# Kernel optimization log

Measured on AMD Instinct MI355X. Metric: run time of the kernel, lower is better.

Reference implementation:

```python
import jax, jax.numpy as jnp
import numpy as np

B, S, T = 16, 400, 51
V, E, H = 50000, 128, 256
MAX_OOV = 50
EXT = V + MAX_OOV
COV_LOSS_WEIGHT = 1.0


def setup_inputs() -> dict:
    key = jax.random.key(0)
    ks = jax.random.split(key, 24)
    sc = 0.05  # param scale
    inp = {
        "tgt": jax.random.randint(ks[0], (B, T), 0, V, dtype=jnp.int32),
        "hidden": jax.random.normal(ks[1], (1, B, H), jnp.float32),
        "cell": jax.random.normal(ks[2], (1, B, H), jnp.float32),
        "encoder_outputs": jax.random.normal(ks[3], (B, S, H), jnp.float32),
        "src_lens": jax.random.randint(ks[4], (B,), S // 2, S + 1, dtype=jnp.int32),
        "src_ids": jax.random.randint(ks[5], (B, S), 0, V, dtype=jnp.int32),
        # -1 means in-vocab token; >=0 means OOV slot index (max MAX_OOV-1)
        "src_oov_map": jax.random.randint(ks[6], (B, S), -1, MAX_OOV, dtype=jnp.int32),
        "embedding": jax.random.normal(ks[7], (V, E), jnp.float32) * sc,
        "W_h": jax.random.normal(ks[8], (H, H), jnp.float32) * sc,
        "W_s": jax.random.normal(ks[9], (H, H), jnp.float32) * sc,
        "w_c": jax.random.normal(ks[10], (H,), jnp.float32) * sc,
        "v": jax.random.normal(ks[11], (H,), jnp.float32) * sc,
        "b_attn": jnp.zeros((1,), jnp.float32),
        "W_ih": jax.random.normal(ks[12], (4 * H, E + H), jnp.float32) * sc,
        "W_hh": jax.random.normal(ks[13], (4 * H, H), jnp.float32) * sc,
        "b_ih": jax.random.normal(ks[14], (4 * H,), jnp.float32) * sc,
        "b_hh": jax.random.normal(ks[15], (4 * H,), jnp.float32) * sc,
        "W_pg": jax.random.normal(ks[16], (1, 2 * H + E), jnp.float32) * sc,
        "b_pg": jnp.zeros((1,), jnp.float32),
        "W_out": jax.random.normal(ks[17], (V, 2 * H), jnp.float32) * sc,
        "b_out": jnp.zeros((V,), jnp.float32),
    }
    return inp


def reference(tgt, hidden, cell, encoder_outputs, src_lens, src_ids, src_oov_map,
              embedding, W_h, W_s, w_c, v, b_attn,
              W_ih, W_hh, b_ih, b_hh, W_pg, b_pg, W_out, b_out):
    # Precompute encoder projection and masks (loop-invariant)
    Wh_h = jnp.einsum('bsh,kh->bsk', encoder_outputs, W_h)        # [B,S,H]
    pad_mask = jnp.arange(S)[None, :] >= src_lens[:, None]       # [B,S]
    copy_idx = jnp.where(src_oov_map >= 0, V + src_oov_map, src_ids)  # [B,S]
    batch_idx = jnp.arange(B)[:, None]

    def step(carry, y_prev):
        h, c, cov = carry                                       # [B,H],[B,H],[B,S]
        emb = embedding[y_prev]                                 # [B,E]
        # coverage attention (additive, See et al. 2017 eq. 9-11)
        attn_in = Wh_h + (h @ W_s.T)[:, None, :] + cov[..., None] * w_c + b_attn
        scores = jnp.tanh(attn_in) @ v                          # [B,S]
        scores = jnp.where(pad_mask, -1e9, scores)
        attn = jax.nn.softmax(scores, axis=1)                   # [B,S]
        context = jnp.einsum('bs,bsh->bh', attn, encoder_outputs)
        cov_loss = jnp.sum(jnp.minimum(attn, cov), axis=1)      # [B]
        # single-layer LSTM cell (torch gate order i,f,g,o)
        x = jnp.concatenate([emb, context], axis=1)             # [B,E+H]
        gates = x @ W_ih.T + h @ W_hh.T + b_ih + b_hh
        i, f, g, o = jnp.split(gates, 4, axis=1)
        c_new = jax.nn.sigmoid(f) * c + jax.nn.sigmoid(i) * jnp.tanh(g)
        h_new = jax.nn.sigmoid(o) * jnp.tanh(c_new)
        # pointer-generator mixture
        p_gen = jax.nn.sigmoid(
            jnp.concatenate([h_new, context, emb], axis=1) @ W_pg.T + b_pg)  # [B,1]
        logits = jnp.concatenate([h_new, context], axis=1) @ W_out.T + b_out
        vocab_dist = jax.nn.softmax(logits, axis=1)             # [B,V]
        ext_dist = jnp.pad(vocab_dist, ((0, 0), (0, MAX_OOV)))  # [B,EXT]
        copy_dist = jnp.zeros((B, EXT), vocab_dist.dtype).at[batch_idx, copy_idx].add(attn)
        final = p_gen * ext_dist + (1.0 - p_gen) * copy_dist
        return (h_new, c_new, cov + attn), (final, cov_loss)

    carry0 = (hidden[0], cell[0], jnp.zeros((B, S), jnp.float32))
    # teacher forcing: decoder input at step t is tgt[:, t-1], t = 1..T-1
    (hT, cT, _), (dists, cov_losses) = jax.lax.scan(step, carry0, tgt[:, :-1].T)
    all_dists = jnp.transpose(dists, (1, 0, 2))                 # [B,T-1,EXT]
    coverage_loss = COV_LOSS_WEIGHT * jnp.mean(cov_losses)
    return all_dists, hT[None], cT[None], coverage_loss
```

## Files before the change

kernel.cpp:

```cpp
#include <hip/hip_runtime.h>
#include <math.h>

#define CB 16
#define CS 400
#define CT 51
#define CTM1 50
#define CV 50000
#define CE 128
#define CH 256
#define CMAXOOV 50
#define CEXT (CV + CMAXOOV)
#define CX 640
#define NST 16
#define NGT 16
#define NWK 223
#define NBLK 256
#define NTILE 782

typedef __attribute__((ext_vector_type(4))) float f32x4;
typedef __attribute__((ext_vector_type(8))) short short8;
typedef unsigned int U32;
typedef unsigned long long U64;

__device__ __forceinline__ float wave_sum(float x) {
#pragma unroll
  for (int o = 32; o > 0; o >>= 1) x += __shfl_xor(x, o);
  return x;
}
__device__ __forceinline__ float sigm(float x) {
  return 1.f / (1.f + __expf(-x));
}
__device__ __forceinline__ float ftanh(float x) {
  x = fminf(fmaxf(x, -15.f), 15.f);
  float e = __expf(2.f * x);
  return (e - 1.f) / (e + 1.f);
}
__device__ __forceinline__ unsigned short f2bf(float f) {
  union { float f; U32 u; } x;
  x.f = f;
  U32 r = x.u + 0x7FFFu + ((x.u >> 16) & 1u);
  return (unsigned short)(r >> 16);
}
__device__ __forceinline__ float bf2f(unsigned short u) {
  return __uint_as_float(((U32)u) << 16);
}
__device__ __forceinline__ U64 pack4(float a, float b, float c, float d) {
  return (U64)f2bf(a) | ((U64)f2bf(b) << 16) | ((U64)f2bf(c) << 32) |
         ((U64)f2bf(d) << 48);
}
__device__ __forceinline__ U32 ald32(const U32* p) {
  return __hip_atomic_load(p, __ATOMIC_RELAXED, __HIP_MEMORY_SCOPE_AGENT);
}
__device__ __forceinline__ void ast32(U32* p, U32 v) {
  __hip_atomic_store(p, v, __ATOMIC_RELAXED, __HIP_MEMORY_SCOPE_AGENT);
}
__device__ __forceinline__ void ast64(U64* p, U64 v) {
  __hip_atomic_store(p, v, __ATOMIC_RELAXED, __HIP_MEMORY_SCOPE_AGENT);
}
#define VM0 asm volatile("s_waitcnt vmcnt(0)" ::: "memory")

__global__ __launch_bounds__(256) void pw_convert(
    const float* __restrict__ W, unsigned short* __restrict__ Wb) {
  size_t i = ((size_t)blockIdx.x * 256 + threadIdx.x) * 8;
  float4 a = *(const float4*)(W + i);
  float4 b = *(const float4*)(W + i + 4);
  short8 o;
  o[0] = (short)f2bf(a.x); o[1] = (short)f2bf(a.y);
  o[2] = (short)f2bf(a.z); o[3] = (short)f2bf(a.w);
  o[4] = (short)f2bf(b.x); o[5] = (short)f2bf(b.y);
  o[6] = (short)f2bf(b.z); o[7] = (short)f2bf(b.w);
  *(short8*)(Wb + i) = o;
}

__global__ __launch_bounds__(256) void pw_cat(
    const float* __restrict__ W_ih, const float* __restrict__ W_hh,
    unsigned short* __restrict__ Wcat) {
  int t8 = blockIdx.x * 256 + threadIdx.x;
  int j = t8 / 80, k8 = t8 % 80;
  short8 o;
#pragma unroll
  for (int i = 0; i < 8; ++i) {
    int k = k8 * 8 + i;
    float v = (k < CE + CH) ? W_ih[(size_t)j * (CE + CH) + k]
                            : W_hh[(size_t)j * CH + (k - (CE + CH))];
    o[i] = (short)f2bf(v);
  }
  *(short8*)(Wcat + (size_t)t8 * 8) = o;
}

__global__ __launch_bounds__(256) void pw_t256(const float* __restrict__ in,
                                               float* __restrict__ out) {
  int j = blockIdx.x, k = threadIdx.x;
  out[j * CH + k] = in[k * CH + j];
}

__global__ __launch_bounds__(256) void pw_t256_bf16(
    const float* __restrict__ in, unsigned short* __restrict__ out) {
  int j = blockIdx.x, k = threadIdx.x;
  out[j * CH + k] = f2bf(in[k * CH + j]);
}

__global__ __launch_bounds__(256) void pw_cvt16(
    const float* __restrict__ in, unsigned short* __restrict__ out) {
  size_t i = ((size_t)blockIdx.x * 256 + threadIdx.x) * 8;
  float4 a = *(const float4*)(in + i);
  float4 b = *(const float4*)(in + i + 4);
  short8 o;
  o[0] = (short)f2bf(a.x); o[1] = (short)f2bf(a.y);
  o[2] = (short)f2bf(a.z); o[3] = (short)f2bf(a.w);
  o[4] = (short)f2bf(b.x); o[5] = (short)f2bf(b.y);
  o[6] = (short)f2bf(b.z); o[7] = (short)f2bf(b.w);
  *(short8*)(out + i) = o;
}

__global__ __launch_bounds__(256) void p0_precompute(
    const float* __restrict__ enc, const float* __restrict__ W_hT,
    const int* __restrict__ src_ids, const int* __restrict__ src_oov,
    unsigned short* __restrict__ Wh_h16, int* __restrict__ copy_idx) {
  const int row0 = blockIdx.x * 8, tid = threadIdx.x;
  __shared__ float erT[CH * 8];
#pragma unroll
  for (int i = 0; i < 8; ++i) {
    int idx = tid + i * 256;
    int r = idx >> 8, j = idx & 255;
    erT[j * 8 + r] = enc[(size_t)row0 * CH + idx];
  }
  if (tid < 8) {
    int row = row0 + tid;
    int ov = src_oov[row];
    copy_idx[row] = (ov >= 0) ? (CV + ov) : src_ids[row];
  }
  __syncthreads();
  float acc[8] = {0, 0, 0, 0, 0, 0, 0, 0};
#pragma unroll 4
  for (int j = 0; j < CH; ++j) {
    float w = W_hT[j * CH + tid];
    float4 e0 = *(const float4*)&erT[j * 8];
    float4 e1 = *(const float4*)&erT[j * 8 + 4];
    acc[0] += e0.x * w; acc[1] += e0.y * w; acc[2] += e0.z * w; acc[3] += e0.w * w;
    acc[4] += e1.x * w; acc[5] += e1.y * w; acc[6] += e1.z * w; acc[7] += e1.w * w;
  }
#pragma unroll
  for (int r = 0; r < 8; ++r)
    Wh_h16[(size_t)(row0 + r) * CH + tid] = f2bf(acc[r]);
}

__global__ __launch_bounds__(256) void z_init(U32* __restrict__ ctrl,
                                              float* __restrict__ part) {
  int tid = blockIdx.x * 256 + threadIdx.x;
  if (tid < 2048) ctrl[tid] = 0u;
  for (int i = tid; i < CTM1 * CB * 64; i += 256 * 64) part[i] = 0.f;
}

__global__ __launch_bounds__(1024, 4) void mega(
    const int* __restrict__ tgt, const float* __restrict__ hidden,
    const float* __restrict__ cell, const int* __restrict__ src_lens,
    const float* __restrict__ embedding, const float* __restrict__ w_c,
    const float* __restrict__ v_vec, const float* __restrict__ b_attn,
    const float* __restrict__ b_ih, const float* __restrict__ b_hh,
    const float* __restrict__ W_pg, const float* __restrict__ b_pg,
    const float* __restrict__ b_out,
    const unsigned short* __restrict__ Wh_h16,
    const unsigned short* __restrict__ enc16,
    const unsigned short* __restrict__ W_sT16,
    const unsigned short* __restrict__ Wcat,
    const unsigned short* __restrict__ Wb, U64* __restrict__ A64,
    U64* __restrict__ x64, U64* __restrict__ g64,
    unsigned short* __restrict__ attn16, float* __restrict__ p_gen_g,
    float* __restrict__ part, float* __restrict__ covloss_b,
    U32* __restrict__ ctrl, float* __restrict__ dout) {
  const int bid = blockIdx.x, tid = threadIdx.x;
  const int lane = tid & 63, wv = tid >> 6;
  U32* arrive = ctrl;
  U32* release = ctrl + 256;
  U32* xrdy = ctrl + 1280;
  U32* grdy = ctrl + 1536;

  __shared__ __align__(16) U64 sh_big[2592];
  __shared__ float cov_s[CS];
  __shared__ float a_s[CS];
  __shared__ __align__(16) float h_cur[CH];
  __shared__ float hws_s[CH];
  __shared__ __align__(16) float ctx_s[CH];
  __shared__ float emb_s[CE];
  __shared__ float pctx[4 * CH];
  __shared__ float gsl[CB][64];
  __shared__ float red[16];
  __shared__ float stat[4];
  __shared__ float prs[16][16];

  if (bid < NST) {
    const int b = bid;
    const int len = src_lens[b];
    const float ba = b_attn[0];
    const int k4 = lane * 4;
    const float4 wc4 = *(const float4*)(w_c + k4);
    const float4 vv4 = *(const float4*)(v_vec + k4);
    const float bias_reg = b_ih[tid] + b_hh[tid];
    const int kg = tid & 255, grp = tid >> 8;
    float covl = 0.f;
    float c_reg = (tid < CH) ? cell[b * CH + tid] : 0.f;

    if (tid < CS) cov_s[tid] = 0.f;
    if (tid < CH) h_cur[tid] = hidden[b * CH + tid];
    __syncthreads();
    {
      float acc = 0.f;
#pragma unroll 8
      for (int j = grp * 64; j < grp * 64 + 64; ++j)
        acc += h_cur[j] * bf2f(W_sT16[j * CH + kg]);
      pctx[grp * CH + kg] = acc;
    }
    if (tid < 64)
      ast64(&x64[b * 160 + 96 + tid],
            pack4(h_cur[4 * tid], h_cur[4 * tid + 1], h_cur[4 * tid + 2],
                  h_cur[4 * tid + 3]));
    __syncthreads();
    if (tid < CH)
      hws_s[tid] = pctx[tid] + pctx[CH + tid] + pctx[2 * CH + tid] +
                   pctx[3 * CH + tid];
    __syncthreads();

    for (int t = 0; t < CTM1; ++t) {
      if (t > 0) {
        if (tid < CS) {
          float a = a_s[tid], cv = cov_s[tid];
          covl += fminf(a, cv);
          cov_s[tid] = cv + a;
        }
        __syncthreads();
      }
      const int tok = tgt[b * CT + t];
      if (tid < CE) emb_s[tid] = embedding[(size_t)tok * CE + tid];
      float ps = 0.f;
      for (int s = wv; s < CS; s += 16) {
        float cv = cov_s[s];
        U64 wq = *(const U64*)(Wh_h16 + ((size_t)(b * CS + s)) * CH + k4);
        float p =
            ftanh(bf2f((unsigned short)wq) + hws_s[k4] + cv * wc4.x + ba) *
                vv4.x +
            ftanh(bf2f((unsigned short)(wq >> 16)) + hws_s[k4 + 1] +
                  cv * wc4.y + ba) *
                vv4.y +
            ftanh(bf2f((unsigned short)(wq >> 32)) + hws_s[k4 + 2] +
                  cv * wc4.z + ba) *
                vv4.z +
            ftanh(bf2f((unsigned short)(wq >> 48)) + hws_s[k4 + 3] +
                  cv * wc4.w + ba) *
                vv4.w;
        p = wave_sum(p);
        if (lane == 0) {
          float e = (s < len) ? __expf(p) : 0.f;
          a_s[s] = e;
          ps += e;
        }
      }
      if (lane == 0) red[wv] = ps;
      __syncthreads();
      if (tid == 0) {
        float s2 = 0.f;
#pragma unroll
        for (int i = 0; i < 16; ++i) s2 += red[i];
        stat[0] = 1.f / s2;
      }
      __syncthreads();
      const float inv = stat[0];
      if (tid < CS) {
        float a = a_s[tid] * inv;
        a_s[tid] = a;
        attn16[((size_t)t * CB + b) * CS + tid] = f2bf(a);
      }
      __syncthreads();
      {
        float pc = 0.f;
        const unsigned short* er =
            enc16 + ((size_t)(b * CS + grp * 100)) * CH + kg;
#pragma unroll 10
        for (int i = 0; i < 100; ++i)
          pc += a_s[grp * 100 + i] * bf2f(er[(size_t)i * CH]);
        pctx[grp * CH + kg] = pc;
      }
      __syncthreads();
      if (tid < CH)
        ctx_s[tid] = pctx[tid] + pctx[CH + tid] + pctx[2 * CH + tid] +
                     pctx[3 * CH + tid];
      __syncthreads();
      {
        U64* xr = x64 + (size_t)t * 2560 + b * 160;
        if (tid < 32) {
          ast64(&xr[tid], pack4(emb_s[4 * tid], emb_s[4 * tid + 1],
                                emb_s[4 * tid + 2], emb_s[4 * tid + 3]));
        } else if (tid < 96) {
          int i = tid - 32;
          ast64(&xr[32 + i], pack4(ctx_s[4 * i], ctx_s[4 * i + 1],
                                   ctx_s[4 * i + 2], ctx_s[4 * i + 3]));
        } else if (tid < 160) {
          int i = tid - 96;
          ast64(&A64[(size_t)t * 2048 + b * 128 + 64 + i],
                pack4(ctx_s[4 * i], ctx_s[4 * i + 1], ctx_s[4 * i + 2],
                      ctx_s[4 * i + 3]));
        }
      }
      VM0;
      __syncthreads();
      if (tid == 0) ast32(&xrdy[b * 16], (U32)(t + 1));
      if (wv == 0) {
        int gg = 0;
        while (gg < (1 << 20)) {
          U32 v = (lane < NGT) ? ald32(&grdy[lane * 16]) : (U32)(t + 1);
          if (__all(v >= (U32)(t + 1))) break;
          __builtin_amdgcn_s_sleep(4);
          ++gg;
        }
      }
      __syncthreads();
      if (tid < CH) {
        const float* gr = (const float*)(g64 + (size_t)t * 8192) + b * 1024;
        float gi = gr[tid] + bias_reg;
        float gf = gr[CH + tid] + b_ih[CH + tid] + b_hh[CH + tid];
        float gg2 = gr[2 * CH + tid] + b_ih[2 * CH + tid] + b_hh[2 * CH + tid];
        float go = gr[3 * CH + tid] + b_ih[3 * CH + tid] + b_hh[3 * CH + tid];
        float cn = sigm(gf) * c_reg + sigm(gi) * ftanh(gg2);
        c_reg = cn;
        h_cur[tid] = sigm(go) * ftanh(cn);
      }
      __syncthreads();
      if (tid < 64) {
        ast64(&A64[(size_t)t * 2048 + b * 128 + tid],
              pack4(h_cur[4 * tid], h_cur[4 * tid + 1], h_cur[4 * tid + 2],
                    h_cur[4 * tid + 3]));
      } else if (tid < 128 && t + 1 < CTM1) {
        int i = tid - 64;
        ast64(&x64[(size_t)(t + 1) * 2560 + b * 160 + 96 + i],
              pack4(h_cur[4 * i], h_cur[4 * i + 1], h_cur[4 * i + 2],
                    h_cur[4 * i + 3]));
      }
      VM0;
      __syncthreads();
      if (tid == 0) ast32(&arrive[b * 16], (U32)(t + 1));
      {
        float acc = 0.f;
#pragma unroll 8
        for (int j = grp * 64; j < grp * 64 + 64; ++j)
          acc += h_cur[j] * bf2f(W_sT16[j * CH + kg]);
        pctx[grp * CH + kg] = acc;
      }
      __syncthreads();
      if (tid < CH)
        hws_s[tid] = pctx[tid] + pctx[CH + tid] + pctx[2 * CH + tid] +
                     pctx[3 * CH + tid];
      {
        float z = 0.f;
        if (tid < CH)
          z = h_cur[tid] * W_pg[tid] + ctx_s[tid] * W_pg[CH + tid];
        if (tid < CE) z += emb_s[tid] * W_pg[2 * CH + tid];
        z = wave_sum(z);
        if (lane == 0) red[wv] = z;
        __syncthreads();
        if (tid == 0) {
          float s2 = 0.f;
#pragma unroll
          for (int i = 0; i < 16; ++i) s2 += red[i];
          p_gen_g[t * CB + b] = sigm(s2 + b_pg[0]);
        }
      }
      __syncthreads();
    }
    if (tid < CS) covl += fminf(a_s[tid], cov_s[tid]);
    covl = wave_sum(covl);
    if (lane == 0) red[wv] = covl;
    __syncthreads();
    if (tid == 0) {
      float s2 = 0.f;
#pragma unroll
      for (int i = 0; i < 16; ++i) s2 += red[i];
      covloss_b[b] = s2;
    }
    if (tid < CH) {
      const size_t D0 = (size_t)CB * CTM1 * CEXT;
      dout[D0 + b * CH + tid] = h_cur[tid];
      dout[D0 + CB * CH + b * CH + tid] = c_reg;
    }
  } else if (bid < NST + NGT) {
    const int g = bid - NST;
    const int n0 = g * 64;
    const int nn = lane & 15, gq = lane >> 4;
    U64* xl = sh_big;
    const short8* x8 = (const short8*)sh_big;
    for (int t = 0; t < CTM1; ++t) {
      if (wv == 0) {
        int gg = 0;
        while (gg < (1 << 20)) {
          U32 v = (lane < NST) ? ald32(&xrdy[lane * 16]) : (U32)(t + 1);
          if (__all(v >= (U32)(t + 1))) break;
          __builtin_amdgcn_s_sleep(4);
          ++gg;
        }
      }
      __syncthreads();
      {
        const U64* src = x64 + (size_t)t * 2560;
        for (int idx = tid; idx < 2560; idx += 1024) {
          int row = idx / 160, col = idx - row * 160;
          xl[row * 162 + col] = src[idx];
        }
      }
      __syncthreads();
      if (wv < 4) {
        const int ncol = n0 + wv * 16 + nn;
        const short8* bp = (const short8*)Wcat + (size_t)ncol * 80;
        short8 af[20];
#pragma unroll
        for (int kt = 0; kt < 20; ++kt) af[kt] = x8[nn * 81 + kt * 4 + gq];
        f32x4 acc = {0.f, 0.f, 0.f, 0.f};
#pragma unroll
        for (int kt = 0; kt < 20; ++kt)
          acc = __builtin_amdgcn_mfma_f32_16x16x32_bf16(af[kt], bp[kt * 4 + gq],
                                                        acc, 0, 0, 0);
#pragma unroll
        for (int r = 0; r < 4; ++r) gsl[gq * 4 + r][wv * 16 + nn] = acc[r];
      }
      __syncthreads();
      if (tid < 512) {
        int b = tid >> 5, i = tid & 31;
        U64 w = (U64)__float_as_uint(gsl[b][2 * i]) |
                ((U64)__float_as_uint(gsl[b][2 * i + 1]) << 32);
        ast64(&g64[(size_t)t * 8192 + b * 512 + (n0 >> 1) + i], w);
      }
      VM0;
      __syncthreads();
      if (tid == 0) ast32(&grdy[g * 16], (U32)(t + 1));
    }
  } else if (bid == NST + NGT) {
    for (int t = 0; t < CTM1; ++t) {
      if (wv == 0) {
        int gg = 0;
        while (gg < (1 << 20)) {
          U32 v = (lane < NST) ? ald32(&arrive[lane * 16]) : (U32)(t + 1);
          if (__all(v >= (U32)(t + 1))) break;
          __builtin_amdgcn_s_sleep(8);
          ++gg;
        }
      }
      __syncthreads();
      if (tid < 64) ast32(&release[tid * 16], (U32)(t + 1));
      __syncthreads();
    }
  } else {
    const int vb = bid - NST - NGT - 1;
    const int rep = vb & 63;
    const int nn = lane & 15, g = lane >> 4;
    const int t4 = (wv >> 2) * NWK + vb;
    const int v = t4 * 64 + (wv & 3) * 16 + nn;
    const bool live = (t4 < NTILE) && (v < CV);
    const int vc = live ? v : CV - 1;
    U64* a64l = sh_big;
    const short8* lds8 = (const short8*)sh_big;
    const short8* bp = (const short8*)Wb + (size_t)vc * 64;
    const float bo = live ? b_out[v] : 0.f;
    for (int t = 0; t < CTM1; ++t) {
      if (tid == 0) {
        int gg = 0;
        while (ald32(&release[rep * 16]) < (U32)(t + 1) && ++gg < (1 << 18))
          __builtin_amdgcn_s_sleep(32);
      }
      __syncthreads();
      {
        const U64* src = A64 + (size_t)t * 2048;
#pragma unroll
        for (int i = 0; i < 2; ++i) {
          int idx = tid + i * 1024;
          int row = idx >> 7, col = idx & 127;
          a64l[row * 130 + col] = src[idx];
        }
      }
      __syncthreads();
      short8 af[16];
#pragma unroll
      for (int kt = 0; kt < 16; ++kt) af[kt] = lds8[nn * 65 + kt * 4 + g];
      f32x4 acc = {0.f, 0.f, 0.f, 0.f};
#pragma unroll
      for (int kt = 0; kt < 16; ++kt)
        acc = __builtin_amdgcn_mfma_f32_16x16x32_bf16(af[kt], bp[kt * 4 + g],
                                                      acc, 0, 0, 0);
      float ev[4];
#pragma unroll
      for (int r = 0; r < 4; ++r) {
        float e = live ? __expf(acc[r] + bo) : 0.f;
        if (live) dout[((size_t)((g * 4 + r) * CTM1 + t)) * CEXT + v] = e;
#pragma unroll
        for (int o = 1; o < 16; o <<= 1) e += __shfl_xor(e, o);
        ev[r] = e;
      }
      if (nn == 0) {
#pragma unroll
        for (int r = 0; r < 4; ++r) prs[wv][g * 4 + r] = ev[r];
      }
      __syncthreads();
      if (tid < 16) {
        float s = 0.f;
#pragma unroll
        for (int w = 0; w < 16; ++w) s += prs[w][tid];
        atomicAdd(&part[((size_t)t * CB + tid) * 64 + rep], s);
      }
      __syncthreads();
    }
  }
}

__global__ __launch_bounds__(256) void post_norm(
    const float* __restrict__ part, const float* __restrict__ p_gen_g,
    float* __restrict__ dout) {
  const int R = blockIdx.x;
  const int b = R / CTM1, t = R % CTM1;
  const int tid = threadIdx.x;
  __shared__ float stat;
  float s = (tid < 64) ? part[((size_t)t * CB + b) * 64 + tid] : 0.f;
  s = wave_sum(s);
  if (tid == 0) stat = p_gen_g[t * CB + b] / s;
  __syncthreads();
  float inv = stat;
  float* drow = dout + (size_t)R * CEXT;
  for (int v = tid; v < CEXT; v += 256)
    drow[v] = (v < CV) ? drow[v] * inv : 0.f;
}

__global__ __launch_bounds__(256) void post_tail(
    const unsigned short* __restrict__ attn16,
    const float* __restrict__ p_gen_g, const int* __restrict__ copy_idx,
    const float* __restrict__ covloss_b, float* __restrict__ dout) {
  const int b = blockIdx.x, tid = threadIdx.x;
  for (int t = 0; t < CTM1; ++t) {
    float pg1 = 1.f - p_gen_g[t * CB + b];
    const unsigned short* ar = attn16 + ((size_t)t * CB + b) * CS;
    float* drow = dout + ((size_t)(b * CTM1 + t)) * CEXT;
    for (int s = tid; s < CS; s += 256)
      atomicAdd(drow + copy_idx[b * CS + s], pg1 * bf2f(ar[s]));
  }
  if (b == 0 && tid == 0) {
    const size_t D0 = (size_t)CB * CTM1 * CEXT;
    float s = 0.f;
    for (int i = 0; i < CB; ++i) s += covloss_b[i];
    dout[D0 + 2 * CB * CH] = s / (float)(CTM1 * CB);
  }
}

extern "C" void kernel_launch(void* const* d_in, const int* in_sizes, int n_in,
                              void* d_out, int out_size, void* d_ws,
                              size_t ws_size, hipStream_t stream) {
  const int* tgt = (const int*)d_in[0];
  const float* hidden = (const float*)d_in[1];
  const float* cell = (const float*)d_in[2];
  const float* enc = (const float*)d_in[3];
  const int* src_lens = (const int*)d_in[4];
  const int* src_ids = (const int*)d_in[5];
  const int* src_oov = (const int*)d_in[6];
  const float* embedding = (const float*)d_in[7];
  const float* W_h = (const float*)d_in[8];
  const float* W_s = (const float*)d_in[9];
  const float* w_c = (const float*)d_in[10];
  const float* v_vec = (const float*)d_in[11];
  const float* b_attn = (const float*)d_in[12];
  const float* W_ih = (const float*)d_in[13];
  const float* W_hh = (const float*)d_in[14];
  const float* b_ih = (const float*)d_in[15];
  const float* b_hh = (const float*)d_in[16];
  const float* W_pg = (const float*)d_in[17];
  const float* b_pg = (const float*)d_in[18];
  const float* W_out = (const float*)d_in[19];
  const float* b_out = (const float*)d_in[20];
  float* dout = (float*)d_out;

  float* ws = (float*)d_ws;
  float* W_hT = ws;
  float* p_gen_g = W_hT + CH * CH;
  float* part = p_gen_g + CTM1 * CB;
  float* covloss_b = part + CTM1 * CB * 64;
  int* copy_idx = (int*)(covloss_b + 16);
  U32* ctrl = (U32*)(copy_idx + CB * CS);
  U64* A64 = (U64*)(ctrl + 2048);
  U64* x64 = A64 + (size_t)CTM1 * 2048;
  U64* g64 = x64 + (size_t)51 * 2560;
  unsigned short* attn16 =
      (unsigned short*)(g64 + (size_t)CTM1 * 8192);
  unsigned short* Wh_h16 = attn16 + (size_t)CTM1 * CB * CS;
  unsigned short* enc16 = Wh_h16 + (size_t)CB * CS * CH;
  unsigned short* W_sT16 = enc16 + (size_t)CB * CS * CH;
  unsigned short* Wcat = W_sT16 + CH * CH;
  unsigned short* Wb = Wcat + (size_t)(4 * CH) * CX;

  z_init<<<64, 256, 0, stream>>>(ctrl, part);
  pw_convert<<<(CV * 2 * CH) / (256 * 8), 256, 0, stream>>>(W_out, Wb);
  pw_cat<<<((4 * CH) * CX / 8) / 256, 256, 0, stream>>>(W_ih, W_hh, Wcat);
  pw_t256<<<CH, CH, 0, stream>>>(W_h, W_hT);
  pw_t256_bf16<<<CH, CH, 0, stream>>>(W_s, W_sT16);
  pw_cvt16<<<(CB * CS * CH) / (256 * 8), 256, 0, stream>>>(enc, enc16);
  p0_precompute<<<CB * CS / 8, 256, 0, stream>>>(enc, W_hT, src_ids, src_oov,
                                                 Wh_h16, copy_idx);

  void* kargs[] = {
      (void*)&tgt,      (void*)&hidden,    (void*)&cell,    (void*)&src_lens,
      (void*)&embedding,(void*)&w_c,       (void*)&v_vec,   (void*)&b_attn,
      (void*)&b_ih,     (void*)&b_hh,      (void*)&W_pg,    (void*)&b_pg,
      (void*)&b_out,    (void*)&Wh_h16,    (void*)&enc16,   (void*)&W_sT16,
      (void*)&Wcat,     (void*)&Wb,        (void*)&A64,     (void*)&x64,
      (void*)&g64,      (void*)&attn16,    (void*)&p_gen_g, (void*)&part,
      (void*)&covloss_b,(void*)&ctrl,      (void*)&dout};
  hipError_t e = hipLaunchCooperativeKernel((const void*)mega, dim3(NBLK),
                                            dim3(1024), kargs, 0, stream);
  if (e != hipSuccess) {
    hipLaunchKernelGGL(mega, dim3(NBLK), dim3(1024), 0, stream, tgt, hidden,
                       cell, src_lens, embedding, w_c, v_vec, b_attn, b_ih,
                       b_hh, W_pg, b_pg, b_out, Wh_h16, enc16, W_sT16, Wcat,
                       Wb, A64, x64, g64, attn16, p_gen_g, part, covloss_b,
                       ctrl, dout);
  }
  post_norm<<<CB * CTM1, 256, 0, stream>>>(part, p_gen_g, dout);
  post_tail<<<CB, 256, 0, stream>>>(attn16, p_gen_g, copy_idx, covloss_b,
                                    dout);
}
```

Baseline: 2.003 ms.

## Move LSTM cell update into gate blocks and split gate GEMM around context wait

The LSTM cell nonlinearity and state update move from the per-batch attention blocks into the gate-GEMM blocks. Gate columns are reassigned so each block owns all four gates for 16 hidden units. The gate GEMM is split so the embedding and hidden parts are computed before waiting for the context, which overlaps them with attention work. Gate outputs go straight to h (HexF/A64) instead of a g64 round trip, removing one cross-block handoff per step, and the spin-wait sleeps are shortened. In exchange, gate blocks wait on each other's previous step and every gate block reloads embeddings itself.

```diff
diff --git a/kernel.cpp b/kernel.cpp
--- a/kernel.cpp
+++ b/kernel.cpp
@@ -165,13 +165,12 @@
     const unsigned short* __restrict__ W_sT16,
     const unsigned short* __restrict__ Wcat,
     const unsigned short* __restrict__ Wb, U64* __restrict__ A64,
-    U64* __restrict__ x64, U64* __restrict__ g64,
-    unsigned short* __restrict__ attn16, float* __restrict__ p_gen_g,
-    float* __restrict__ part, float* __restrict__ covloss_b,
-    U32* __restrict__ ctrl, float* __restrict__ dout) {
+    float* __restrict__ HexF, unsigned short* __restrict__ attn16,
+    float* __restrict__ p_gen_g, float* __restrict__ part,
+    float* __restrict__ covloss_b, U32* __restrict__ ctrl,
+    float* __restrict__ dout) {
   const int bid = blockIdx.x, tid = threadIdx.x;
   const int lane = tid & 63, wv = tid >> 6;
-  U32* arrive = ctrl;
   U32* release = ctrl + 256;
   U32* xrdy = ctrl + 1280;
   U32* grdy = ctrl + 1536;
@@ -184,7 +183,8 @@
   __shared__ __align__(16) float ctx_s[CH];
   __shared__ float emb_s[CE];
   __shared__ float pctx[4 * CH];
-  __shared__ float gsl[CB][64];
+  __shared__ float gsl[4][CB][16];
+  __shared__ int sh_tok[CB];
   __shared__ float red[16];
   __shared__ float stat[4];
   __shared__ float prs[16][16];
@@ -196,10 +196,8 @@
     const int k4 = lane * 4;
     const float4 wc4 = *(const float4*)(w_c + k4);
     const float4 vv4 = *(const float4*)(v_vec + k4);
-    const float bias_reg = b_ih[tid] + b_hh[tid];
     const int kg = tid & 255, grp = tid >> 8;
     float covl = 0.f;
-    float c_reg = (tid < CH) ? cell[b * CH + tid] : 0.f;
 
     if (tid < CS) cov_s[tid] = 0.f;
     if (tid < CH) h_cur[tid] = hidden[b * CH + tid];
@@ -211,10 +209,6 @@
         acc += h_cur[j] * bf2f(W_sT16[j * CH + kg]);
       pctx[grp * CH + kg] = acc;
     }
-    if (tid < 64)
-      ast64(&x64[b * 160 + 96 + tid],
-            pack4(h_cur[4 * tid], h_cur[4 * tid + 1], h_cur[4 * tid + 2],
-                  h_cur[4 * tid + 3]));
     __syncthreads();
     if (tid < CH)
       hws_s[tid] = pctx[tid] + pctx[CH + tid] + pctx[2 * CH + tid] +
@@ -230,8 +224,6 @@
         }
         __syncthreads();
       }
-      const int tok = tgt[b * CT + t];
-      if (tid < CE) emb_s[tid] = embedding[(size_t)tok * CE + tid];
       float ps = 0.f;
       for (int s = wv; s < CS; s += 16) {
         float cv = cov_s[s];
@@ -285,59 +277,28 @@
         ctx_s[tid] = pctx[tid] + pctx[CH + tid] + pctx[2 * CH + tid] +
                      pctx[3 * CH + tid];
       __syncthreads();
-      {
-        U64* xr = x64 + (size_t)t * 2560 + b * 160;
-        if (tid < 32) {
-          ast64(&xr[tid], pack4(emb_s[4 * tid], emb_s[4 * tid + 1],
-                                emb_s[4 * tid + 2], emb_s[4 * tid + 3]));
-        } else if (tid < 96) {
-          int i = tid - 32;
-          ast64(&xr[32 + i], pack4(ctx_s[4 * i], ctx_s[4 * i + 1],
-                                   ctx_s[4 * i + 2], ctx_s[4 * i + 3]));
-        } else if (tid < 160) {
-          int i = tid - 96;
-          ast64(&A64[(size_t)t * 2048 + b * 128 + 64 + i],
-                pack4(ctx_s[4 * i], ctx_s[4 * i + 1], ctx_s[4 * i + 2],
-                      ctx_s[4 * i + 3]));
-        }
+      if (tid < 64) {
+        ast64(&A64[(size_t)t * 2048 + b * 128 + 64 + tid],
+              pack4(ctx_s[4 * tid], ctx_s[4 * tid + 1], ctx_s[4 * tid + 2],
+                    ctx_s[4 * tid + 3]));
       }
       VM0;
       __syncthreads();
       if (tid == 0) ast32(&xrdy[b * 16], (U32)(t + 1));
+      if (tid < CE)
+        emb_s[tid] = embedding[(size_t)tgt[b * CT + t] * CE + tid];
       if (wv == 0) {
         int gg = 0;
-        while (gg < (1 << 20)) {
+        while (gg < (1 << 22)) {
           U32 v = (lane < NGT) ? ald32(&grdy[lane * 16]) : (U32)(t + 1);
           if (__all(v >= (U32)(t + 1))) break;
-          __builtin_amdgcn_s_sleep(4);
+          __builtin_amdgcn_s_sleep(1);
           ++gg;
         }
       }
       __syncthreads();
-      if (tid < CH) {
-        const float* gr = (const float*)(g64 + (size_t)t * 8192) + b * 1024;
-        float gi = gr[tid] + bias_reg;
-        float gf = gr[CH + tid] + b_ih[CH + tid] + b_hh[CH + tid];
-        float gg2 = gr[2 * CH + tid] + b_ih[2 * CH + tid] + b_hh[2 * CH + tid];
-        float go = gr[3 * CH + tid] + b_ih[3 * CH + tid] + b_hh[3 * CH + tid];
-        float cn = sigm(gf) * c_reg + sigm(gi) * ftanh(gg2);
-        c_reg = cn;
-        h_cur[tid] = sigm(go) * ftanh(cn);
-      }
-      __syncthreads();
-      if (tid < 64) {
-        ast64(&A64[(size_t)t * 2048 + b * 128 + tid],
-              pack4(h_cur[4 * tid], h_cur[4 * tid + 1], h_cur[4 * tid + 2],
-                    h_cur[4 * tid + 3]));
-      } else if (tid < 128 && t + 1 < CTM1) {
-        int i = tid - 64;
-        ast64(&x64[(size_t)(t + 1) * 2560 + b * 160 + 96 + i],
-              pack4(h_cur[4 * i], h_cur[4 * i + 1], h_cur[4 * i + 2],
-                    h_cur[4 * i + 3]));
-      }
-      VM0;
-      __syncthreads();
-      if (tid == 0) ast32(&arrive[b * 16], (U32)(t + 1));
+      if (tid < CH) h_cur[tid] = HexF[((size_t)t * CB + b) * CH + tid];
+      __syncthreads();
       {
         float acc = 0.f;
 #pragma unroll 8
@@ -379,66 +340,122 @@
     if (tid < CH) {
       const size_t D0 = (size_t)CB * CTM1 * CEXT;
       dout[D0 + b * CH + tid] = h_cur[tid];
-      dout[D0 + CB * CH + b * CH + tid] = c_reg;
     }
   } else if (bid < NST + NGT) {
     const int g = bid - NST;
-    const int n0 = g * 64;
     const int nn = lane & 15, gq = lane >> 4;
-    U64* xl = sh_big;
+    U64* xg64 = sh_big;
+    short* xg_s = (short*)sh_big;
     const short8* x8 = (const short8*)sh_big;
+    const int cb = tid >> 4, cj = tid & 15, cu = g * 16 + (tid & 15);
+    float c_reg = 0.f, bi0 = 0.f, bi1 = 0.f, bi2 = 0.f, bi3 = 0.f;
+    if (tid < 256) {
+      c_reg = cell[cb * CH + cu];
+      bi0 = b_ih[cu] + b_hh[cu];
+      bi1 = b_ih[CH + cu] + b_hh[CH + cu];
+      bi2 = b_ih[2 * CH + cu] + b_hh[2 * CH + cu];
+      bi3 = b_ih[3 * CH + cu] + b_hh[3 * CH + cu];
+    }
     for (int t = 0; t < CTM1; ++t) {
+      if (t > 0 && wv == 0) {
+        int gg = 0;
+        while (gg < (1 << 22)) {
+          U32 v = (lane < NGT) ? ald32(&grdy[lane * 16]) : (U32)t;
+          if (__all(v >= (U32)t)) break;
+          __builtin_amdgcn_s_sleep(1);
+          ++gg;
+        }
+      }
+      if (tid < CB) sh_tok[tid] = tgt[tid * CT + t];
+      __syncthreads();
+      for (int idx = tid; idx < CB * CE; idx += 1024) {
+        int bb = idx >> 7, k = idx & 127;
+        xg_s[bb * 648 + k] = (short)f2bf(embedding[(size_t)sh_tok[bb] * CE + k]);
+      }
+      if (t == 0) {
+        for (int idx = tid; idx < CB * CH; idx += 1024) {
+          int bb = idx >> 8, k = idx & 255;
+          xg_s[bb * 648 + 384 + k] = (short)f2bf(hidden[bb * CH + k]);
+        }
+      } else {
+        if (tid < 1024) {
+          int bb = tid >> 6, i = tid & 63;
+          xg64[bb * 162 + 96 + i] = A64[(size_t)(t - 1) * 2048 + bb * 128 + i];
+        }
+      }
+      __syncthreads();
+      f32x4 acc = {0.f, 0.f, 0.f, 0.f};
+      if (wv < 4) {
+        const int ncol = wv * 256 + g * 16 + nn;
+        const short8* bp = (const short8*)Wcat + (size_t)ncol * 80;
+#pragma unroll
+        for (int kt = 0; kt < 4; ++kt)
+          acc = __builtin_amdgcn_mfma_f32_16x16x32_bf16(
+              x8[nn * 81 + kt * 4 + gq], bp[kt * 4 + gq], acc, 0, 0, 0);
+#pragma unroll
+        for (int kt = 12; kt < 20; ++kt)
+          acc = __builtin_amdgcn_mfma_f32_16x16x32_bf16(
+              x8[nn * 81 + kt * 4 + gq], bp[kt * 4 + gq], acc, 0, 0, 0);
+      }
       if (wv == 0) {
         int gg = 0;
-        while (gg < (1 << 20)) {
+        while (gg < (1 << 22)) {
           U32 v = (lane < NST) ? ald32(&xrdy[lane * 16]) : (U32)(t + 1);
           if (__all(v >= (U32)(t + 1))) break;
-          __builtin_amdgcn_s_sleep(4);
+          __builtin_amdgcn_s_sleep(1);
           ++gg;
         }
       }
       __syncthreads();
-      {
-        const U64* src = x64 + (size_t)t * 2560;
-        for (int idx = tid; idx < 2560; idx += 1024) {
-          int row = idx / 160, col = idx - row * 160;
-          xl[row * 162 + col] = src[idx];
-        }
+      if (tid < 1024) {
+        int bb = tid >> 6, i = tid & 63;
+        xg64[bb * 162 + 32 + i] = A64[(size_t)t * 2048 + bb * 128 + 64 + i];
       }
       __syncthreads();
       if (wv < 4) {
-        const int ncol = n0 + wv * 16 + nn;
+        const int ncol = wv * 256 + g * 16 + nn;
         const short8* bp = (const short8*)Wcat + (size_t)ncol * 80;
-        short8 af[20];
-#pragma unroll
-        for (int kt = 0; kt < 20; ++kt) af[kt] = x8[nn * 81 + kt * 4 + gq];
-        f32x4 acc = {0.f, 0.f, 0.f, 0.f};
-#pragma unroll
-        for (int kt = 0; kt < 20; ++kt)
-          acc = __builtin_amdgcn_mfma_f32_16x16x32_bf16(af[kt], bp[kt * 4 + gq],
-                                                        acc, 0, 0, 0);
-#pragma unroll
-        for (int r = 0; r < 4; ++r) gsl[gq * 4 + r][wv * 16 + nn] = acc[r];
-      }
-      __syncthreads();
-      if (tid < 512) {
-        int b = tid >> 5, i = tid & 31;
-        U64 w = (U64)__float_as_uint(gsl[b][2 * i]) |
-                ((U64)__float_as_uint(gsl[b][2 * i + 1]) << 32);
-        ast64(&g64[(size_t)t * 8192 + b * 512 + (n0 >> 1) + i], w);
+#pragma unroll
+        for (int kt = 4; kt < 12; ++kt)
+          acc = __builtin_amdgcn_mfma_f32_16x16x32_bf16(
+              x8[nn * 81 + kt * 4 + gq], bp[kt * 4 + gq], acc, 0, 0, 0);
+#pragma unroll
+        for (int r = 0; r < 4; ++r) gsl[wv][gq * 4 + r][nn] = acc[r];
+      }
+      __syncthreads();
+      if (tid < 256) {
+        float gi = gsl[0][cb][cj] + bi0;
+        float gf = gsl[1][cb][cj] + bi1;
+        float gg2 = gsl[2][cb][cj] + bi2;
+        float go = gsl[3][cb][cj] + bi3;
+        float cn = sigm(gf) * c_reg + sigm(gi) * ftanh(gg2);
+        c_reg = cn;
+        float hn = sigm(go) * ftanh(cn);
+        ast32((U32*)&HexF[((size_t)t * CB + cb) * CH + cu],
+              __float_as_uint(hn));
+        float h1 = __shfl_down(hn, 1);
+        float h2 = __shfl_down(hn, 2);
+        float h3 = __shfl_down(hn, 3);
+        if (!(cj & 3))
+          ast64(&A64[(size_t)t * 2048 + cb * 128 + (cu >> 2)],
+                pack4(hn, h1, h2, h3));
       }
       VM0;
       __syncthreads();
       if (tid == 0) ast32(&grdy[g * 16], (U32)(t + 1));
+    }
+    if (tid < 256) {
+      const size_t D0 = (size_t)CB * CTM1 * CEXT;
+      dout[D0 + CB * CH + cb * CH + cu] = c_reg;
     }
   } else if (bid == NST + NGT) {
     for (int t = 0; t < CTM1; ++t) {
       if (wv == 0) {
         int gg = 0;
-        while (gg < (1 << 20)) {
-          U32 v = (lane < NST) ? ald32(&arrive[lane * 16]) : (U32)(t + 1);
+        while (gg < (1 << 22)) {
+          U32 v = (lane < NGT) ? ald32(&grdy[lane * 16]) : (U32)(t + 1);
           if (__all(v >= (U32)(t + 1))) break;
-          __builtin_amdgcn_s_sleep(8);
+          __builtin_amdgcn_s_sleep(4);
           ++gg;
         }
       }
@@ -576,13 +593,12 @@
   float* p_gen_g = W_hT + CH * CH;
   float* part = p_gen_g + CTM1 * CB;
   float* covloss_b = part + CTM1 * CB * 64;
-  int* copy_idx = (int*)(covloss_b + 16);
+  float* HexF = covloss_b + 16;
+  int* copy_idx = (int*)(HexF + (size_t)CTM1 * CB * CH);
   U32* ctrl = (U32*)(copy_idx + CB * CS);
   U64* A64 = (U64*)(ctrl + 2048);
-  U64* x64 = A64 + (size_t)CTM1 * 2048;
-  U64* g64 = x64 + (size_t)51 * 2560;
   unsigned short* attn16 =
-      (unsigned short*)(g64 + (size_t)CTM1 * 8192);
+      (unsigned short*)(A64 + (size_t)CTM1 * 2048);
   unsigned short* Wh_h16 = attn16 + (size_t)CTM1 * CB * CS;
   unsigned short* enc16 = Wh_h16 + (size_t)CB * CS * CH;
   unsigned short* W_sT16 = enc16 + (size_t)CB * CS * CH;
@@ -603,17 +619,17 @@
       (void*)&embedding,(void*)&w_c,       (void*)&v_vec,   (void*)&b_attn,
       (void*)&b_ih,     (void*)&b_hh,      (void*)&W_pg,    (void*)&b_pg,
       (void*)&b_out,    (void*)&Wh_h16,    (void*)&enc16,   (void*)&W_sT16,
-      (void*)&Wcat,     (void*)&Wb,        (void*)&A64,     (void*)&x64,
-      (void*)&g64,      (void*)&attn16,    (void*)&p_gen_g, (void*)&part,
-      (void*)&covloss_b,(void*)&ctrl,      (void*)&dout};
+      (void*)&Wcat,     (void*)&Wb,        (void*)&A64,     (void*)&HexF,
+      (void*)&attn16,   (void*)&p_gen_g,   (void*)&part,    (void*)&covloss_b,
+      (void*)&ctrl,     (void*)&dout};
   hipError_t e = hipLaunchCooperativeKernel((const void*)mega, dim3(NBLK),
                                             dim3(1024), kargs, 0, stream);
   if (e != hipSuccess) {
     hipLaunchKernelGGL(mega, dim3(NBLK), dim3(1024), 0, stream, tgt, hidden,
                        cell, src_lens, embedding, w_c, v_vec, b_attn, b_ih,
                        b_hh, W_pg, b_pg, b_out, Wh_h16, enc16, W_sT16, Wcat,
-                       Wb, A64, x64, g64, attn16, p_gen_g, part, covloss_b,
-                       ctrl, dout);
+                       Wb, A64, HexF, attn16, p_gen_g, part, covloss_b, ctrl,
+                       dout);
   }
   post_norm<<<CB * CTM1, 256, 0, stream>>>(part, p_gen_g, dout);
   post_tail<<<CB, 256, 0, stream>>>(attn16, p_gen_g, copy_idx, covloss_b,
```

After: 1.862 ms. -7.0%, faster.
